# Kernel tuning notes

Measured on AMD Instinct MI355X. Metric: run time of the kernel, lower is better.

Reference implementation:

```python
import jax, jax.numpy as jnp
import numpy as np

H = 12      # heads
P = 4       # dim_point
CHUNK = 256 # chunk_size
DIM_SINGLE = 768
DIM_PAIR = 64
B, N = 1, 1024


def setup_inputs() -> dict:
    key = jax.random.key(0)
    ks = jax.random.split(key, 24)
    s = 0.02
    d = DIM_SINGLE
    inp = {
        'single': jax.random.normal(ks[0], (B, N, d), jnp.float32),
        'pair': jax.random.normal(ks[1], (B, N, N, DIM_PAIR), jnp.float32),
        'rot': jax.random.normal(ks[2], (B, N, 3, 3), jnp.float32),
        'trans': jax.random.normal(ks[3], (B, N, 3), jnp.float32),
        # Linear weights stored as (in, out) so y = x @ W + b
        'Wq': jax.random.normal(ks[4], (d, d), jnp.float32) * s,
        'bq': jnp.zeros((d,), jnp.float32),
        'Wk': jax.random.normal(ks[5], (d, d), jnp.float32) * s,
        'bk': jnp.zeros((d,), jnp.float32),
        'Wv': jax.random.normal(ks[6], (d, d), jnp.float32) * s,
        'bv': jnp.zeros((d,), jnp.float32),
        'Wpb': jax.random.normal(ks[7], (DIM_PAIR, H), jnp.float32) * s,
        'bpb': jnp.zeros((H,), jnp.float32),
        'Wqp': jax.random.normal(ks[8], (d, H * P * 3), jnp.float32) * s,
        'bqp': jnp.zeros((H * P * 3,), jnp.float32),
        'Wkp': jax.random.normal(ks[9], (d, H * P * 3), jnp.float32) * s,
        'bkp': jnp.zeros((H * P * 3,), jnp.float32),
        'Wvp': jax.random.normal(ks[10], (d, H * P * 3), jnp.float32) * s,
        'bvp': jnp.zeros((H * P * 3,), jnp.float32),
        'Wo': jax.random.normal(ks[11], (d, d), jnp.float32) * s,
        'bo': jnp.zeros((d,), jnp.float32),
        'Wpo': jax.random.normal(ks[12], (H * P * 3, d), jnp.float32) * s,
        'bpo': jnp.zeros((d,), jnp.float32),
        'ln_g': jnp.ones((d,), jnp.float32),
        'ln_b': jnp.zeros((d,), jnp.float32),
    }
    return inp


def _layernorm(x, g, b, eps=1e-5):
    mu = jnp.mean(x, axis=-1, keepdims=True)
    var = jnp.mean((x - mu) ** 2, axis=-1, keepdims=True)
    return (x - mu) * jax.lax.rsqrt(var + eps) * g + b


def reference(single, pair, rot, trans, Wq, bq, Wk, bk, Wv, bv, Wpb, bpb,
              Wqp, bqp, Wkp, bkp, Wvp, bvp, Wo, bo, Wpo, bpo, ln_g, ln_b):
    Bs, Ns, C = single.shape
    Ch = C // H
    scale = Ch ** (-0.5)

    q = (single @ Wq + bq).reshape(Bs, Ns, H, Ch)
    k = (single @ Wk + bk).reshape(Bs, Ns, H, Ch)
    v = (single @ Wv + bv).reshape(Bs, Ns, H, Ch)

    # [B,N,N,H] -> [B,H,N,M]
    pair_bias = jnp.transpose(pair @ Wpb + bpb, (0, 3, 1, 2))

    q_pts = (single @ Wqp + bqp).reshape(Bs, Ns, H, P, 3)
    k_pts = (single @ Wkp + bkp).reshape(Bs, Ns, H, P, 3)
    v_pts = (single @ Wvp + bvp).reshape(Bs, Ns, H, P, 3)

    t = trans[:, :, None, None, :]  # [B,N,1,1,3]
    q_pts_g = jnp.einsum('bnhpd,bnde->bnhpe', q_pts, rot) + t
    k_pts_g = jnp.einsum('bnhpd,bnde->bnhpe', k_pts, rot) + t
    v_pts_g = jnp.einsum('bnhpd,bnde->bnhpe', v_pts, rot) + t

    q2_h = jnp.transpose(jnp.sum(q_pts_g ** 2, axis=(3, 4)), (0, 2, 1))  # [B,H,N]
    k2_h = jnp.transpose(jnp.sum(k_pts_g ** 2, axis=(3, 4)), (0, 2, 1))  # [B,H,N]

    scalar_logits = jnp.einsum('bnhc,bmhc->bhnm', q, k) * scale  # [B,H,N,N]

    out_scalar = jnp.zeros((Bs, Ns, H, Ch), single.dtype)
    out_points = jnp.zeros((Bs, Ns, H, P, 3), single.dtype)

    # Faithful to the original: softmax is taken PER CHUNK over the key axis,
    # and the per-chunk weighted sums are accumulated.
    for start in range(0, Ns, CHUNK):
        end = min(start + CHUNK, Ns)
        qk = jnp.einsum('bnhpd,bmhpd->bhnm', q_pts_g, k_pts_g[:, start:end])
        pt_logits = -0.5 * (q2_h[:, :, :, None] + k2_h[:, :, None, start:end]
                            - 2.0 * qk) * scale
        logits = scalar_logits[:, :, :, start:end] + pair_bias[:, :, :, start:end] + pt_logits
        attn = jax.nn.softmax(logits, axis=-1)  # [B,H,N,chunk]
        out_scalar = out_scalar + jnp.einsum('bhnm,bmhc->bnhc', attn, v[:, start:end])
        out_points = out_points + jnp.einsum('bhnm,bmhpd->bnhpd', attn, v_pts_g[:, start:end])

    weighted_scalar = out_scalar.reshape(Bs, Ns, H * Ch)
    weighted_points = out_points.reshape(Bs, Ns, H * P * 3)
    point_proj = weighted_points @ Wpo + bpo
    out = (weighted_scalar + point_proj) @ Wo + bo
    return _layernorm(single + out, ln_g, ln_b)
```

## Files before the change

### kernel.cpp

```cpp
#include <hip/hip_runtime.h>
#include <hip/hip_bf16.h>
#include <stdint.h>

#define NTOK 1024
#define NH 12
#define QPSLAB 2801664

typedef short bf16x8 __attribute__((ext_vector_type(8)));
typedef float f32x4 __attribute__((ext_vector_type(4)));
typedef uint32_t u32x4 __attribute__((ext_vector_type(4)));

__device__ __forceinline__ unsigned short f2bf(float f) {
  union { float f; uint32_t u; } x; x.f = f;
  uint32_t r = x.u + 0x7FFFu + ((x.u >> 16) & 1u);
  return (unsigned short)(r >> 16);
}
__device__ __forceinline__ float bf2f(unsigned short u) {
  union { uint32_t u; float f; } x; x.u = ((uint32_t)u) << 16;
  return x.f;
}
__device__ __forceinline__ bf16x8 pack8(float4 a, float4 b) {
  union { __hip_bfloat162 h2[4]; bf16x8 v; } u;
  u.h2[0] = __float22bfloat162_rn(make_float2(a.x, a.y));
  u.h2[1] = __float22bfloat162_rn(make_float2(a.z, a.w));
  u.h2[2] = __float22bfloat162_rn(make_float2(b.x, b.y));
  u.h2[3] = __float22bfloat162_rn(make_float2(b.z, b.w));
  return u.v;
}

__global__ __launch_bounds__(256) void fat1_k(
    const float* __restrict__ pair, const float* __restrict__ Wpb,
    const float* __restrict__ bpb, unsigned short* __restrict__ pb,
    const float* __restrict__ single, const float* __restrict__ Wq,
    const float* __restrict__ Wk, const float* __restrict__ Wv,
    const float* __restrict__ Wqp, const float* __restrict__ Wkp,
    const float* __restrict__ Wvp, const float* __restrict__ Wpo,
    const float* __restrict__ Wo,
    const float* __restrict__ bq, const float* __restrict__ bk,
    const float* __restrict__ bv, const float* __restrict__ bqp,
    const float* __restrict__ bkp, const float* __restrict__ bvp,
    unsigned short* __restrict__ sgl, unsigned short* __restrict__ wcat,
    unsigned short* __restrict__ WB, unsigned short* __restrict__ wpoA,
    float* __restrict__ bcat)
{
  __shared__ char smem[12288];
  const int bid = blockIdx.x, t = threadIdx.x;

  if (bid < 4096) {
    unsigned short* wpbt = (unsigned short*)smem;
    for (int i = t; i < 1024; i += 256) {
      int h = i >> 6, k = i & 63;
      wpbt[i] = (h < 12) ? f2bf(Wpb[k * 12 + h]) : (unsigned short)0;
    }
    __syncthreads();
    const int w = t >> 6, lane = t & 63;
    const int lr = lane & 15, g = lane >> 4;
    unsigned short* stg = (unsigned short*)(smem + 2048) + w * 960;
    bf16x8 wf0 = *(const bf16x8*)(wpbt + lr * 64 + g * 8);
    bf16x8 wf1 = *(const bf16x8*)(wpbt + lr * 64 + 32 + g * 8);
    const float bias_h = (lr < 12) ? bpb[lr] : 0.f;
    const int wid = bid * 4 + w;
#pragma unroll
    for (int it = 0; it < 4; ++it) {
      int nm0 = (wid * 4 + it) * 16;
      const float* src = pair + (size_t)(nm0 + lr) * 64 + g * 8;
      float4 aA = *(const float4*)(src);
      float4 aB = *(const float4*)(src + 4);
      float4 aC = *(const float4*)(src + 32);
      float4 aD = *(const float4*)(src + 36);
      bf16x8 f0 = pack8(aA, aB);
      bf16x8 f1 = pack8(aC, aD);
      f32x4 c = {0.f, 0.f, 0.f, 0.f};
      c = __builtin_amdgcn_mfma_f32_16x16x32_bf16(f0, wf0, c, 0, 0, 0);
      c = __builtin_amdgcn_mfma_f32_16x16x32_bf16(f1, wf1, c, 0, 0, 0);
      if (lr < 12) {
        union { __hip_bfloat162 h2[2]; ushort4 s4; } pu;
        pu.h2[0] = __float22bfloat162_rn(make_float2(c[0] + bias_h, c[1] + bias_h));
        pu.h2[1] = __float22bfloat162_rn(make_float2(c[2] + bias_h, c[3] + bias_h));
        *(ushort4*)(stg + lr * 80 + it * 16 + g * 4) = pu.s4;
      }
    }
    {
      const int h0 = lane >> 3, c0 = lane & 7;
      u32x4 v0 = *(const u32x4*)(stg + h0 * 80 + c0 * 8);
      *(u32x4*)(pb + (((size_t)h0) << 20) + (size_t)wid * 64 + c0 * 8) = v0;
      if (lane < 32) {
        int h1 = 8 + h0;
        u32x4 v1 = *(const u32x4*)(stg + h1 * 80 + c0 * 8);
        *(u32x4*)(pb + (((size_t)h1) << 20) + (size_t)wid * 64 + c0 * 8) = v1;
      }
    }
    return;
  }

  int b = bid - 4096;
  if (b < 2628) {
    unsigned short (*tl)[72] = (unsigned short(*)[72])smem;
    const float* src; unsigned short* dst; int N, dstld, rowbase;
    if (b < 1728) {
      int j = b / 576; b -= j * 576;
      src = (j == 0) ? Wq : (j == 1) ? Wk : Wv;
      N = 768; dst = wcat; dstld = 768; rowbase = j * 768;
    } else if (b < 2052) {
      b -= 1728; int j = b / 108; b -= j * 108;
      src = (j == 0) ? Wqp : (j == 1) ? Wkp : Wvp;
      N = 144; dst = wcat; dstld = 768; rowbase = 2304 + j * 144;
    } else {
      b -= 2052; src = Wo; N = 768; dst = WB; dstld = 912; rowbase = 0;
    }
    const int k0 = (b % 12) * 64, n0 = (b / 12) * 16;
#pragma unroll
    for (int i = 0; i < 4; ++i) {
      int kk = (t >> 4) + i * 16;
      int nn = t & 15;
      tl[nn][kk] = f2bf(src[(size_t)(k0 + kk) * N + n0 + nn]);
    }
    __syncthreads();
#pragma unroll
    for (int i = 0; i < 4; ++i) {
      int kk = t & 63;
      int nn = (t >> 6) + i * 4;
      dst[(size_t)(rowbase + n0 + nn) * dstld + k0 + kk] = tl[nn][kk];
    }
    return;
  }
  if (b < 3396) {
    int i = (b - 2628) * 256 + t;
    float4 v = *(const float4*)(single + (size_t)i * 4);
    ushort4 o;
    o.x = f2bf(v.x); o.y = f2bf(v.y); o.z = f2bf(v.z); o.w = f2bf(v.w);
    *(ushort4*)(sgl + (size_t)i * 4) = o;
    return;
  }
  if (b < 3504) {
    int i = (b - 3396) * 256 + t;
    float4 v = *(const float4*)(Wpo + (size_t)i * 4);
    ushort4 o;
    o.x = f2bf(v.x); o.y = f2bf(v.y); o.z = f2bf(v.z); o.w = f2bf(v.w);
    *(ushort4*)(wpoA + (size_t)i * 4) = o;
    return;
  }
  {
    int idx = (b - 3504) * 256 + t;
    if (idx < 2736) {
      float v;
      if (idx < 768) v = bq[idx];
      else if (idx < 1536) v = bk[idx - 768];
      else if (idx < 2304) v = bv[idx - 1536];
      else if (idx < 2448) v = bqp[idx - 2304];
      else if (idx < 2592) v = bkp[idx - 2448];
      else v = bvp[idx - 2592];
      bcat[idx] = v;
    }
  }
}

template <int EPI>
__device__ __forceinline__ void gemm_dev(
    unsigned short* As, unsigned short* Bs,
    const unsigned short* __restrict__ A, int lda, int Mact,
    const unsigned short* __restrict__ Bt, int ldb, int Nact,
    int kt0, int ktn, int kmax,
    float* __restrict__ outf, unsigned short* __restrict__ outb, int ldc,
    const float* __restrict__ p0, int mb, int nb, int addbias)
{
  const int t = threadIdx.x;
  const int w = t >> 6, lane = t & 63;
  const int wr = w >> 1, wc = w & 1;
  const int lr = lane & 15, lc = lane >> 4;
  const int m0 = mb * 128, n0 = nb * 128;
  const int r0 = t >> 2, c0 = t & 3;
  const int r1 = r0 + 64;

  f32x4 acc[4][4] = {};
  u32x4 zz = {0u, 0u, 0u, 0u};
  u32x4 pa0, pa1, pq0, pq1;

#define LOAD_AB(KT)                                                              \
  do {                                                                           \
    int k0_ = (KT) * 32;                                                         \
    int g0_ = k0_ + c0 * 8;                                                      \
    pa0 = (g0_ < kmax && (m0 + r0) < Mact)                                       \
              ? *(const u32x4*)(A + (size_t)(m0 + r0) * lda + g0_) : zz;         \
    pa1 = (g0_ < kmax && (m0 + r1) < Mact)                                       \
              ? *(const u32x4*)(A + (size_t)(m0 + r1) * lda + g0_) : zz;         \
    pq0 = (g0_ < kmax && (n0 + r0) < Nact)                                       \
              ? *(const u32x4*)(Bt + (size_t)(n0 + r0) * ldb + g0_) : zz;        \
    pq1 = (g0_ < kmax && (n0 + r1) < Nact)                                       \
              ? *(const u32x4*)(Bt + (size_t)(n0 + r1) * ldb + g0_) : zz;        \
  } while (0)

  LOAD_AB(kt0);
  for (int kt = kt0; kt < kt0 + ktn; ++kt) {
    __syncthreads();
    ((u32x4*)As)[r0 * 4 + c0] = pa0;
    ((u32x4*)As)[r1 * 4 + c0] = pa1;
    ((u32x4*)Bs)[r0 * 4 + c0] = pq0;
    ((u32x4*)Bs)[r1 * 4 + c0] = pq1;
    __syncthreads();
    if (kt + 1 < kt0 + ktn) LOAD_AB(kt + 1);

    bf16x8 af[4], bfr[4];
#pragma unroll
    for (int mi = 0; mi < 4; ++mi) {
      int row = wr * 64 + mi * 16 + lr;
      af[mi] = *(const bf16x8*)(As + (row * 4 + lc) * 8);
    }
#pragma unroll
    for (int ni = 0; ni < 4; ++ni) {
      int row = wc * 64 + ni * 16 + lr;
      bfr[ni] = *(const bf16x8*)(Bs + (row * 4 + lc) * 8);
    }
#pragma unroll
    for (int mi = 0; mi < 4; ++mi)
#pragma unroll
      for (int ni = 0; ni < 4; ++ni)
        acc[mi][ni] = __builtin_amdgcn_mfma_f32_16x16x32_bf16(
            af[mi], bfr[ni], acc[mi][ni], 0, 0, 0);
  }
#undef LOAD_AB

#pragma unroll
  for (int mi = 0; mi < 4; ++mi) {
#pragma unroll
    for (int ni = 0; ni < 4; ++ni) {
#pragma unroll
      for (int r = 0; r < 4; ++r) {
        int row = m0 + wr * 64 + mi * 16 + lc * 4 + r;
        int col = n0 + wc * 64 + ni * 16 + lr;
        if (row < Mact && col < Nact) {
          float v = acc[mi][ni][r];
          if constexpr (EPI == 0) {
            outf[(size_t)row * ldc + col] = addbias ? (v + p0[col]) : v;
          } else {
            outb[(size_t)col * 912 + 768 + row] = f2bf(v);
          }
        }
      }
    }
  }
}

__global__ __launch_bounds__(256) void fat2_k(
    const unsigned short* __restrict__ sgl, const unsigned short* __restrict__ wcat,
    const float* __restrict__ bcat, float* __restrict__ qp2,
    const unsigned short* __restrict__ wpoA, unsigned short* __restrict__ WB,
    const float* __restrict__ bpo, const float* __restrict__ Wo,
    const float* __restrict__ bo, float* __restrict__ bfused)
{
  __shared__ unsigned short As[128 * 32];
  __shared__ unsigned short Bs[128 * 32];
  const int bid = blockIdx.x;
  const int t = threadIdx.x;

  if (bid < 12) {
    int mb = bid & 1, nb = bid >> 1;
    gemm_dev<1>(As, Bs, wpoA, 768, 144, WB, 912, 768, 0, 24, 768,
                nullptr, WB, 912, nullptr, mb, nb, 0);
    return;
  }
  if (bid < 15) {
    int n = (bid - 12) * 256 + t;
    float sacc = bo[n];
    for (int j = 0; j < 768; ++j) sacc += bpo[j] * Wo[(size_t)j * 768 + n];
    bfused[n] = sacc;
    return;
  }
  {
    int pbid = bid - 15;
    int zk = pbid / 176, rem = pbid % 176;
    int mb = rem & 7, nb = rem >> 3;
    gemm_dev<0>(As, Bs, sgl, 768, 1024, wcat, 768, 2736,
                zk * 12, 12, 768,
                qp2 + (size_t)zk * QPSLAB, nullptr, 2736, bcat, mb, nb, zk == 0);
  }
}

__global__ __launch_bounds__(256) void rotate_k(
    const float* __restrict__ qp2, const float* __restrict__ rot,
    const float* __restrict__ trans,
    unsigned short* __restrict__ Acat, unsigned short* __restrict__ Bcat,
    unsigned short* __restrict__ VcatT, float* __restrict__ q2k2)
{
  const int n = blockIdx.x, t = threadIdx.x;
  __shared__ float R[9], T[3], rg[432];
  if (t < 9) R[t] = rot[n * 9 + t];
  if (t >= 9 && t < 12) T[t - 9] = trans[n * 3 + (t - 9)];
  __syncthreads();
  for (int s = t; s < 432; s += 256) {
    int j = s / 144, r = s % 144;
    int h = r / 12, wo = r % 12;
    int e = wo % 3;
    size_t base = (size_t)n * 2736 + 2304 + j * 144 + (r - e);
    float d0 = qp2[base + 0] + qp2[base + 0 + QPSLAB];
    float d1 = qp2[base + 1] + qp2[base + 1 + QPSLAB];
    float d2 = qp2[base + 2] + qp2[base + 2 + QPSLAB];
    float val = d0 * R[e] + d1 * R[3 + e] + d2 * R[6 + e] + T[e];
    rg[s] = val;
    unsigned short bv = f2bf(val);
    if (j == 0)      Acat[((size_t)h * NTOK + n) * 96 + 64 + wo] = bv;
    else if (j == 1) Bcat[((size_t)h * NTOK + n) * 96 + 64 + wo] = bv;
    else             VcatT[((size_t)h * 80 + 64 + wo) * NTOK + n] = bv;
  }
  __syncthreads();
  for (int s = t; s < 2304; s += 256) {
    int j = s / 768, c = s % 768;
    int h = c >> 6, cc = c & 63;
    size_t ix = (size_t)n * 2736 + s;
    unsigned short bv = f2bf(qp2[ix] + qp2[ix + QPSLAB]);
    if (j == 0)      Acat[((size_t)h * NTOK + n) * 96 + cc] = bv;
    else if (j == 1) Bcat[((size_t)h * NTOK + n) * 96 + cc] = bv;
    else             VcatT[((size_t)h * 80 + cc) * NTOK + n] = bv;
  }
  if (t < 240) {
    int h = t / 20, ix = 76 + t % 20;
    Acat[((size_t)h * NTOK + n) * 96 + ix] = 0;
    Bcat[((size_t)h * NTOK + n) * 96 + ix] = 0;
  }
  if (t >= 240 && t < 288) {
    int s = t - 240;
    int h = s / 4, rr = 76 + s % 4;
    VcatT[((size_t)h * 80 + rr) * NTOK + n] = 0;
  }
  if (t < 24) {
    int j = t / 12, h = t % 12;
    float sum = 0.f;
#pragma unroll
    for (int wo = 0; wo < 12; ++wo) {
      float v = rg[j * 144 + h * 12 + wo];
      sum += v * v;
    }
    q2k2[(size_t)(j * NH + h) * NTOK + n] = sum;
  }
}

__global__ __launch_bounds__(256) void attn_k(
    const unsigned short* __restrict__ pb, const unsigned short* __restrict__ Acat,
    const unsigned short* __restrict__ Bcat, const unsigned short* __restrict__ VcatT,
    const float* __restrict__ q2k2, float* __restrict__ acc4)
{
  __shared__ unsigned short Ls[64 * 256];
  __shared__ unsigned short Bs[128 * 104];
  const int t = threadIdx.x, w = t >> 6, lane = t & 63;
  const int lr = lane & 15, lc = lane >> 4;
  const int n0 = blockIdx.x * 64;
  const int m0 = blockIdx.y * 256;
  const int h  = blockIdx.z;

  const unsigned short* Pg = pb + ((size_t)h << 20) + (size_t)n0 * 1024 + m0;
#pragma unroll
  for (int i = 0; i < 8; ++i) {
    int idx = i * 256 + t;
    int row = idx >> 5, sl = idx & 31;
    u32x4 v = *(const u32x4*)(Pg + (size_t)row * 1024 + sl * 8);
    ((u32x4*)Ls)[row * 32 + (sl ^ (row & 7))] = v;
  }
  const unsigned short* Kg = Bcat + ((size_t)h * 1024 + m0) * 96;
#pragma unroll
  for (int i = 0; i < 6; ++i) {
    int idx = i * 256 + t;
    int row = idx / 12, c = idx % 12;
    u32x4 v = *(const u32x4*)(Kg + (size_t)row * 96 + c * 8);
    *(u32x4*)(Bs + row * 104 + c * 8) = v;
  }
  __syncthreads();

  bf16x8 qf[3];
  const unsigned short* Qg = Acat + ((size_t)h * 1024 + n0 + w * 16 + lr) * 96;
#pragma unroll
  for (int kk = 0; kk < 3; ++kk) qf[kk] = *(const bf16x8*)(Qg + kk * 32 + lc * 8);

  f32x4 sa[16];
#pragma unroll
  for (int ct = 0; ct < 16; ++ct) sa[ct] = (f32x4){0.f, 0.f, 0.f, 0.f};

#pragma unroll
  for (int ct = 0; ct < 8; ++ct)
#pragma unroll
    for (int kk = 0; kk < 3; ++kk) {
      bf16x8 kf = *(const bf16x8*)(Bs + (ct * 16 + lr) * 104 + kk * 32 + lc * 8);
      sa[ct] = __builtin_amdgcn_mfma_f32_16x16x32_bf16(kf, qf[kk], sa[ct], 0, 0, 0);
    }
  __syncthreads();
#pragma unroll
  for (int i = 0; i < 6; ++i) {
    int idx = i * 256 + t;
    int row = idx / 12, c = idx % 12;
    u32x4 v = *(const u32x4*)(Kg + (size_t)(128 + row) * 96 + c * 8);
    *(u32x4*)(Bs + row * 104 + c * 8) = v;
  }
  __syncthreads();
#pragma unroll
  for (int ct = 8; ct < 16; ++ct)
#pragma unroll
    for (int kk = 0; kk < 3; ++kk) {
      bf16x8 kf = *(const bf16x8*)(Bs + ((ct - 8) * 16 + lr) * 104 + kk * 32 + lc * 8);
      sa[ct] = __builtin_amdgcn_mfma_f32_16x16x32_bf16(kf, qf[kk], sa[ct], 0, 0, 0);
    }

  const int nrow = w * 16 + lr;
  const float q2v = q2k2[(size_t)h * 1024 + n0 + nrow];
  const float* k2b = q2k2 + 12288 + (size_t)h * 1024 + m0;
  float mx = -1e30f;
#pragma unroll
  for (int ct = 0; ct < 16; ++ct) {
    int sl = (ct * 2 + (lc >> 1)) ^ (nrow & 7);
    const unsigned short* p = Ls + nrow * 256 + sl * 8 + (lc & 1) * 4;
    ushort4 pv = *(const ushort4*)p;
    float4 k2v = *(const float4*)(k2b + ct * 16 + lc * 4);
    sa[ct][0] = 0.125f * sa[ct][0] + bf2f(pv.x) - 0.0625f * (q2v + k2v.x);
    sa[ct][1] = 0.125f * sa[ct][1] + bf2f(pv.y) - 0.0625f * (q2v + k2v.y);
    sa[ct][2] = 0.125f * sa[ct][2] + bf2f(pv.z) - 0.0625f * (q2v + k2v.z);
    sa[ct][3] = 0.125f * sa[ct][3] + bf2f(pv.w) - 0.0625f * (q2v + k2v.w);
    mx = fmaxf(mx, fmaxf(fmaxf(sa[ct][0], sa[ct][1]), fmaxf(sa[ct][2], sa[ct][3])));
  }
  mx = fmaxf(mx, __shfl_xor(mx, 16, 64));
  mx = fmaxf(mx, __shfl_xor(mx, 32, 64));
  float sm = 0.f;
#pragma unroll
  for (int ct = 0; ct < 16; ++ct)
#pragma unroll
    for (int r = 0; r < 4; ++r) { sa[ct][r] = __expf(sa[ct][r] - mx); sm += sa[ct][r]; }
  sm += __shfl_xor(sm, 16, 64);
  sm += __shfl_xor(sm, 32, 64);
  float inv = 1.0f / sm;
#pragma unroll
  for (int ct = 0; ct < 16; ++ct) {
    int sl = (ct * 2 + (lc >> 1)) ^ (nrow & 7);
    unsigned short* p = Ls + nrow * 256 + sl * 8 + (lc & 1) * 4;
    union { __hip_bfloat162 h2[2]; ushort4 s4; } pu;
    pu.h2[0] = __float22bfloat162_rn(make_float2(sa[ct][0] * inv, sa[ct][1] * inv));
    pu.h2[1] = __float22bfloat162_rn(make_float2(sa[ct][2] * inv, sa[ct][3] * inv));
    *(ushort4*)p = pu.s4;
  }
  __syncthreads();

  f32x4 acc[5];
#pragma unroll
  for (int nf = 0; nf < 5; ++nf) acc[nf] = (f32x4){0.f, 0.f, 0.f, 0.f};
  const unsigned short* Vg = VcatT + (size_t)h * 80 * NTOK + m0;
#pragma unroll
  for (int kk = 0; kk < 8; ++kk) {
    int row = w * 16 + lr;
    int sl = (kk * 4 + lc) ^ (row & 7);
    bf16x8 a = *(const bf16x8*)(Ls + row * 256 + sl * 8);
#pragma unroll
    for (int nf = 0; nf < 5; ++nf) {
      int c = nf * 16 + lr;
      bf16x8 b = *(const bf16x8*)(Vg + (size_t)c * NTOK + kk * 32 + lc * 8);
      acc[nf] = __builtin_amdgcn_mfma_f32_16x16x32_bf16(a, b, acc[nf], 0, 0, 0);
    }
  }
  float* out = acc4 + ((size_t)blockIdx.y * NH + h) * (size_t)NTOK * 80;
#pragma unroll
  for (int nf = 0; nf < 5; ++nf)
#pragma unroll
    for (int r = 0; r < 4; ++r) {
      int orow = n0 + w * 16 + lc * 4 + r;
      int c = nf * 16 + lr;
      out[(size_t)orow * 80 + c] = acc[nf][r];
    }
}

__global__ __launch_bounds__(256) void reduce_k(
    const float* __restrict__ acc4, unsigned short* __restrict__ AW)
{
  int idx = blockIdx.x * 256 + threadIdx.x;
  if (idx >= 1024 * 912) return;
  int n = idx / 912, c = idx % 912;
  const size_t cs = (size_t)NH * NTOK * 80;
  size_t base;
  if (c < 768) {
    int h = c >> 6, cc = c & 63;
    base = ((size_t)h * NTOK + n) * 80 + cc;
  } else {
    int c2 = c - 768;
    int h = c2 / 12, wo = c2 % 12;
    base = ((size_t)h * NTOK + n) * 80 + 64 + wo;
  }
  float v = acc4[base] + acc4[base + cs] + acc4[base + 2 * cs] + acc4[base + 3 * cs];
  AW[(size_t)n * 912 + c] = f2bf(v);
}

__global__ __launch_bounds__(256) void tail_gemm_k(
    const unsigned short* __restrict__ AW, const unsigned short* __restrict__ WB,
    float* __restrict__ outpre)
{
  __shared__ unsigned short As[128 * 32];
  __shared__ unsigned short Bs[128 * 32];
  int z = blockIdx.z;
  int kt0 = z * 8, ktn = (z < 3) ? 8 : 5;
  gemm_dev<0>(As, Bs, AW, 912, 1024, WB, 912, 768, kt0, ktn, 912,
              outpre + (size_t)z * 786432, nullptr, 768, nullptr,
              blockIdx.x, blockIdx.y, 0);
}

__global__ __launch_bounds__(256) void ln_k(
    const float* __restrict__ single, const float* __restrict__ outpre,
    const float* __restrict__ bfused, const float* __restrict__ g,
    const float* __restrict__ b, float* __restrict__ out)
{
  const int row = blockIdx.x, t = threadIdx.x;
  __shared__ float red[8];
  size_t base = (size_t)row * 768;
  const size_t SL = 786432;
  float x[3];
#pragma unroll
  for (int j = 0; j < 3; ++j) {
    int c = t + j * 256;
    float v = single[base + c] + bfused[c];
#pragma unroll
    for (int z = 0; z < 4; ++z) v += outpre[base + c + (size_t)z * SL];
    x[j] = v;
  }
  float s = x[0] + x[1] + x[2];
#pragma unroll
  for (int off = 32; off; off >>= 1) s += __shfl_xor(s, off, 64);
  if ((t & 63) == 0) red[t >> 6] = s;
  __syncthreads();
  float mu = (red[0] + red[1] + red[2] + red[3]) * (1.0f / 768.0f);
  float d0 = x[0] - mu, d1 = x[1] - mu, d2 = x[2] - mu;
  float vs = d0 * d0 + d1 * d1 + d2 * d2;
#pragma unroll
  for (int off = 32; off; off >>= 1) vs += __shfl_xor(vs, off, 64);
  if ((t & 63) == 0) red[4 + (t >> 6)] = vs;
  __syncthreads();
  float var = (red[4] + red[5] + red[6] + red[7]) * (1.0f / 768.0f);
  float rs = rsqrtf(var + 1e-5f);
  out[base + t]       = d0 * rs * g[t]       + b[t];
  out[base + t + 256] = d1 * rs * g[t + 256] + b[t + 256];
  out[base + t + 512] = d2 * rs * g[t + 512] + b[t + 512];
}

extern "C" void kernel_launch(void* const* d_in, const int* in_sizes, int n_in,
                              void* d_out, int out_size, void* d_ws, size_t ws_size,
                              hipStream_t stream)
{
  (void)in_sizes; (void)n_in; (void)out_size; (void)ws_size;
  const float* single = (const float*)d_in[0];
  const float* pair   = (const float*)d_in[1];
  const float* rot    = (const float*)d_in[2];
  const float* trans  = (const float*)d_in[3];
  const float* Wq  = (const float*)d_in[4];  const float* bq  = (const float*)d_in[5];
  const float* Wk  = (const float*)d_in[6];  const float* bk  = (const float*)d_in[7];
  const float* Wv  = (const float*)d_in[8];  const float* bv  = (const float*)d_in[9];
  const float* Wpb = (const float*)d_in[10]; const float* bpb = (const float*)d_in[11];
  const float* Wqp = (const float*)d_in[12]; const float* bqp = (const float*)d_in[13];
  const float* Wkp = (const float*)d_in[14]; const float* bkp = (const float*)d_in[15];
  const float* Wvp = (const float*)d_in[16]; const float* bvp = (const float*)d_in[17];
  const float* Wo  = (const float*)d_in[18]; const float* bo  = (const float*)d_in[19];
  const float* Wpo = (const float*)d_in[20]; const float* bpo = (const float*)d_in[21];
  const float* lng = (const float*)d_in[22]; const float* lnb = (const float*)d_in[23];

  char* ws = (char*)d_ws;
  unsigned short* sgl    = (unsigned short*)(ws + 0);
  unsigned short* wcat   = (unsigned short*)(ws + 1572864);
  unsigned short* wpoA   = (unsigned short*)(ws + 5775360);
  unsigned short* WB     = (unsigned short*)(ws + 5996544);
  float*          bcat   = (float*)(ws + 7397376);
  float*          bfused = (float*)(ws + 7410432);
  float*          qp2    = (float*)(ws + 7413504);
  unsigned short* Acat   = (unsigned short*)(ws + 29826816);
  unsigned short* Bcat   = (unsigned short*)(ws + 32186112);
  unsigned short* VcatT  = (unsigned short*)(ws + 34545408);
  float*          q2k2   = (float*)(ws + 36511488);
  unsigned short* pb     = (unsigned short*)(ws + 36609792);
  float*          acc4   = (float*)(ws + 61775616);
  unsigned short* AW     = (unsigned short*)(ws + 77504256);
  float*          outpre = (float*)(ws + 79372032);

  fat1_k<<<7611, 256, 0, stream>>>(pair, Wpb, bpb, pb,
                                   single, Wq, Wk, Wv, Wqp, Wkp, Wvp, Wpo, Wo,
                                   bq, bk, bv, bqp, bkp, bvp,
                                   sgl, wcat, WB, wpoA, bcat);

  fat2_k<<<367, 256, 0, stream>>>(sgl, wcat, bcat, qp2, wpoA, WB,
                                  bpo, Wo, bo, bfused);

  rotate_k<<<1024, 256, 0, stream>>>(qp2, rot, trans, Acat, Bcat, VcatT, q2k2);

  attn_k<<<dim3(16, 4, 12), 256, 0, stream>>>(pb, Acat, Bcat, VcatT, q2k2, acc4);

  reduce_k<<<3648, 256, 0, stream>>>(acc4, AW);

  tail_gemm_k<<<dim3(8, 6, 4), 256, 0, stream>>>(AW, WB, outpre);

  ln_k<<<1024, 256, 0, stream>>>(single, outpre, bfused, lng, lnb, (float*)d_out);
}
```

Measured before the change: 186.3 us.

## Split pair-bias projection across first three kernels to overlap with projection work

The pair-bias projection (a 256MB read of pair) was done entirely in the first fused kernel. It is now split into four quarters: one runs in the prep kernel, two run alongside the QKV projection GEMM, and one runs alongside the rotate kernel. The goal is to fill the idle CUs in the small GEMM and rotate launches with bandwidth-bound work. The per-wave code also drops the LDS weight staging and the staged coalesced store, loading Wpb per lane and writing 8-byte stores straight to pb. Those stores are less coalesced, and the redundant Wpb loads add some cost.

Measured after the change: 195.5 us. 1.05x slower.

```diff
diff --git a/kernel.cpp b/kernel.cpp
--- a/kernel.cpp
+++ b/kernel.cpp
@@ -28,7 +28,47 @@
   return u.v;
 }
 
-__global__ __launch_bounds__(256) void fat1_k(
+__device__ __forceinline__ void pb_wave(
+    const float* __restrict__ pair, const float* __restrict__ Wpb,
+    const float* __restrict__ bpb, unsigned short* __restrict__ pb,
+    int wid, int t)
+{
+  const int lane = t & 63;
+  const int lr = lane & 15, g = lane >> 4;
+  bf16x8 wf0 = {0, 0, 0, 0, 0, 0, 0, 0};
+  bf16x8 wf1 = {0, 0, 0, 0, 0, 0, 0, 0};
+  float bias_h = 0.f;
+  if (lr < 12) {
+#pragma unroll
+    for (int j = 0; j < 8; ++j) {
+      wf0[j] = (short)f2bf(Wpb[(g * 8 + j) * 12 + lr]);
+      wf1[j] = (short)f2bf(Wpb[(32 + g * 8 + j) * 12 + lr]);
+    }
+    bias_h = bpb[lr];
+  }
+#pragma unroll
+  for (int it = 0; it < 4; ++it) {
+    int nm0 = (wid * 4 + it) * 16;
+    const float* src = pair + (size_t)(nm0 + lr) * 64 + g * 8;
+    float4 aA = *(const float4*)(src);
+    float4 aB = *(const float4*)(src + 4);
+    float4 aC = *(const float4*)(src + 32);
+    float4 aD = *(const float4*)(src + 36);
+    bf16x8 f0 = pack8(aA, aB);
+    bf16x8 f1 = pack8(aC, aD);
+    f32x4 c = {0.f, 0.f, 0.f, 0.f};
+    c = __builtin_amdgcn_mfma_f32_16x16x32_bf16(f0, wf0, c, 0, 0, 0);
+    c = __builtin_amdgcn_mfma_f32_16x16x32_bf16(f1, wf1, c, 0, 0, 0);
+    if (lr < 12) {
+      union { __hip_bfloat162 h2[2]; ushort4 s4; } pu;
+      pu.h2[0] = __float22bfloat162_rn(make_float2(c[0] + bias_h, c[1] + bias_h));
+      pu.h2[1] = __float22bfloat162_rn(make_float2(c[2] + bias_h, c[3] + bias_h));
+      *(ushort4*)(pb + ((size_t)lr << 20) + (size_t)nm0 + g * 4) = pu.s4;
+    }
+  }
+}
+
+__global__ __launch_bounds__(256) void k1_pb0_prep(
     const float* __restrict__ pair, const float* __restrict__ Wpb,
     const float* __restrict__ bpb, unsigned short* __restrict__ pb,
     const float* __restrict__ single, const float* __restrict__ Wq,
@@ -43,59 +83,14 @@
     unsigned short* __restrict__ WB, unsigned short* __restrict__ wpoA,
     float* __restrict__ bcat)
 {
-  __shared__ char smem[12288];
   const int bid = blockIdx.x, t = threadIdx.x;
-
-  if (bid < 4096) {
-    unsigned short* wpbt = (unsigned short*)smem;
-    for (int i = t; i < 1024; i += 256) {
-      int h = i >> 6, k = i & 63;
-      wpbt[i] = (h < 12) ? f2bf(Wpb[k * 12 + h]) : (unsigned short)0;
-    }
-    __syncthreads();
-    const int w = t >> 6, lane = t & 63;
-    const int lr = lane & 15, g = lane >> 4;
-    unsigned short* stg = (unsigned short*)(smem + 2048) + w * 960;
-    bf16x8 wf0 = *(const bf16x8*)(wpbt + lr * 64 + g * 8);
-    bf16x8 wf1 = *(const bf16x8*)(wpbt + lr * 64 + 32 + g * 8);
-    const float bias_h = (lr < 12) ? bpb[lr] : 0.f;
-    const int wid = bid * 4 + w;
-#pragma unroll
-    for (int it = 0; it < 4; ++it) {
-      int nm0 = (wid * 4 + it) * 16;
-      const float* src = pair + (size_t)(nm0 + lr) * 64 + g * 8;
-      float4 aA = *(const float4*)(src);
-      float4 aB = *(const float4*)(src + 4);
-      float4 aC = *(const float4*)(src + 32);
-      float4 aD = *(const float4*)(src + 36);
-      bf16x8 f0 = pack8(aA, aB);
-      bf16x8 f1 = pack8(aC, aD);
-      f32x4 c = {0.f, 0.f, 0.f, 0.f};
-      c = __builtin_amdgcn_mfma_f32_16x16x32_bf16(f0, wf0, c, 0, 0, 0);
-      c = __builtin_amdgcn_mfma_f32_16x16x32_bf16(f1, wf1, c, 0, 0, 0);
-      if (lr < 12) {
-        union { __hip_bfloat162 h2[2]; ushort4 s4; } pu;
-        pu.h2[0] = __float22bfloat162_rn(make_float2(c[0] + bias_h, c[1] + bias_h));
-        pu.h2[1] = __float22bfloat162_rn(make_float2(c[2] + bias_h, c[3] + bias_h));
-        *(ushort4*)(stg + lr * 80 + it * 16 + g * 4) = pu.s4;
-      }
-    }
-    {
-      const int h0 = lane >> 3, c0 = lane & 7;
-      u32x4 v0 = *(const u32x4*)(stg + h0 * 80 + c0 * 8);
-      *(u32x4*)(pb + (((size_t)h0) << 20) + (size_t)wid * 64 + c0 * 8) = v0;
-      if (lane < 32) {
-        int h1 = 8 + h0;
-        u32x4 v1 = *(const u32x4*)(stg + h1 * 80 + c0 * 8);
-        *(u32x4*)(pb + (((size_t)h1) << 20) + (size_t)wid * 64 + c0 * 8) = v1;
-      }
-    }
-    return;
-  }
-
-  int b = bid - 4096;
+  if (bid < 1024) {
+    pb_wave(pair, Wpb, bpb, pb, bid * 16 + 0 + (t >> 6), t);
+    return;
+  }
+  int b = bid - 1024;
   if (b < 2628) {
-    unsigned short (*tl)[72] = (unsigned short(*)[72])smem;
+    __shared__ unsigned short tl[16][72];
     const float* src; unsigned short* dst; int N, dstld, rowbase;
     if (b < 1728) {
       int j = b / 576; b -= j * 576;
@@ -241,33 +236,40 @@
   }
 }
 
-__global__ __launch_bounds__(256) void fat2_k(
+__global__ __launch_bounds__(256) void k2_pb12_proj(
+    const float* __restrict__ pair, const float* __restrict__ Wpb,
+    const float* __restrict__ bpb, unsigned short* __restrict__ pb,
     const unsigned short* __restrict__ sgl, const unsigned short* __restrict__ wcat,
     const float* __restrict__ bcat, float* __restrict__ qp2,
     const unsigned short* __restrict__ wpoA, unsigned short* __restrict__ WB,
     const float* __restrict__ bpo, const float* __restrict__ Wo,
     const float* __restrict__ bo, float* __restrict__ bfused)
 {
+  const int bid = blockIdx.x, t = threadIdx.x;
+  if (bid < 2048) {
+    int grp = 1 + (bid >> 10);
+    int lb  = bid & 1023;
+    pb_wave(pair, Wpb, bpb, pb, lb * 16 + grp * 4 + (t >> 6), t);
+    return;
+  }
   __shared__ unsigned short As[128 * 32];
   __shared__ unsigned short Bs[128 * 32];
-  const int bid = blockIdx.x;
-  const int t = threadIdx.x;
-
-  if (bid < 12) {
-    int mb = bid & 1, nb = bid >> 1;
+  int rb = bid - 2048;
+  if (rb < 12) {
+    int mb = rb & 1, nb = rb >> 1;
     gemm_dev<1>(As, Bs, wpoA, 768, 144, WB, 912, 768, 0, 24, 768,
                 nullptr, WB, 912, nullptr, mb, nb, 0);
     return;
   }
-  if (bid < 15) {
-    int n = (bid - 12) * 256 + t;
+  if (rb < 15) {
+    int n = (rb - 12) * 256 + t;
     float sacc = bo[n];
     for (int j = 0; j < 768; ++j) sacc += bpo[j] * Wo[(size_t)j * 768 + n];
     bfused[n] = sacc;
     return;
   }
   {
-    int pbid = bid - 15;
+    int pbid = rb - 15;
     int zk = pbid / 176, rem = pbid % 176;
     int mb = rem & 7, nb = rem >> 3;
     gemm_dev<0>(As, Bs, sgl, 768, 1024, wcat, 768, 2736,
@@ -276,13 +278,20 @@
   }
 }
 
-__global__ __launch_bounds__(256) void rotate_k(
+__global__ __launch_bounds__(256) void k3_pb3_rotate(
+    const float* __restrict__ pair, const float* __restrict__ Wpb,
+    const float* __restrict__ bpb, unsigned short* __restrict__ pb,
     const float* __restrict__ qp2, const float* __restrict__ rot,
     const float* __restrict__ trans,
     unsigned short* __restrict__ Acat, unsigned short* __restrict__ Bcat,
     unsigned short* __restrict__ VcatT, float* __restrict__ q2k2)
 {
-  const int n = blockIdx.x, t = threadIdx.x;
+  const int bid = blockIdx.x, t = threadIdx.x;
+  if (bid < 1024) {
+    pb_wave(pair, Wpb, bpb, pb, bid * 16 + 12 + (t >> 6), t);
+    return;
+  }
+  const int n = bid - 1024;
   __shared__ float R[9], T[3], rg[432];
   if (t < 9) R[t] = rot[n * 9 + t];
   if (t >= 9 && t < 12) T[t - 9] = trans[n * 3 + (t - 9)];
@@ -569,15 +578,17 @@
   unsigned short* AW     = (unsigned short*)(ws + 77504256);
   float*          outpre = (float*)(ws + 79372032);
 
-  fat1_k<<<7611, 256, 0, stream>>>(pair, Wpb, bpb, pb,
-                                   single, Wq, Wk, Wv, Wqp, Wkp, Wvp, Wpo, Wo,
-                                   bq, bk, bv, bqp, bkp, bvp,
-                                   sgl, wcat, WB, wpoA, bcat);
-
-  fat2_k<<<367, 256, 0, stream>>>(sgl, wcat, bcat, qp2, wpoA, WB,
-                                  bpo, Wo, bo, bfused);
-
-  rotate_k<<<1024, 256, 0, stream>>>(qp2, rot, trans, Acat, Bcat, VcatT, q2k2);
+  k1_pb0_prep<<<4539, 256, 0, stream>>>(pair, Wpb, bpb, pb,
+                                        single, Wq, Wk, Wv, Wqp, Wkp, Wvp, Wpo, Wo,
+                                        bq, bk, bv, bqp, bkp, bvp,
+                                        sgl, wcat, WB, wpoA, bcat);
+
+  k2_pb12_proj<<<2415, 256, 0, stream>>>(pair, Wpb, bpb, pb,
+                                         sgl, wcat, bcat, qp2, wpoA, WB,
+                                         bpo, Wo, bo, bfused);
+
+  k3_pb3_rotate<<<2048, 256, 0, stream>>>(pair, Wpb, bpb, pb,
+                                          qp2, rot, trans, Acat, Bcat, VcatT, q2k2);
 
   attn_k<<<dim3(16, 4, 12), 256, 0, stream>>>(pb, Acat, Bcat, VcatT, q2k2, acc4);
 
```
